# Kernel tuning notes

Hardware: AMD Instinct MI355X
Metric: run time of the kernel (lower is better)

The kernel has to match this reference:

```python
import jax, jax.numpy as jnp
import numpy as np

# Config constants (HNet300MConfig)
D = 1536          # d_model
H = 12            # n_heads // 2 used by chunk_attention
MAXC = 256        # max_chunks
MAXSEQ = 1024     # max_seq_length (size_embedding rows)
THRESH = 0.85     # boundary_threshold
B, S = 8, 1024


def setup_inputs() -> dict:
    key = jax.random.key(0)
    ks = jax.random.split(key, 10)
    def nrm(k, shape, scale=0.02):
        return jax.random.normal(k, shape, dtype=jnp.float32) * scale
    return {
        "x": jax.random.normal(ks[0], (B, S, D), dtype=jnp.float32),
        "boundaries": jax.random.uniform(ks[1], (B, S), dtype=jnp.float32),
        # nn.MultiheadAttention params
        "in_proj_w": nrm(ks[2], (3 * D, D)),
        "in_proj_b": jnp.zeros((3 * D,), jnp.float32),
        "out_w": nrm(ks[3], (D, D)),
        "out_b": jnp.zeros((D,), jnp.float32),
        # chunk_processor: Linear(D,2D) -> GELU -> Linear(2D,D) -> LayerNorm
        "w1": nrm(ks[4], (2 * D, D)),
        "b1": jnp.zeros((2 * D,), jnp.float32),
        "w2": nrm(ks[5], (D, 2 * D)),
        "b2": jnp.zeros((D,), jnp.float32),
        "ln_g": jnp.ones((D,), jnp.float32),
        "ln_b": jnp.zeros((D,), jnp.float32),
        "pos_enc": nrm(ks[6], (1, MAXC, D)),         # chunk_pos_encoding
        "size_emb": nrm(ks[7], (MAXSEQ, D), 1.0),    # size_embedding table
    }


def reference(x, boundaries, in_proj_w, in_proj_b, out_w, out_b,
              w1, b1, w2, b2, ln_g, ln_b, pos_enc, size_emb):
    dh = D // H
    # Chunk structure: boundary positions start chunks; seg_id = #boundaries up to
    # and including this token, minus 1. Tokens before the first boundary (seg=-1)
    # belong to no chunk. Final chunk runs from last boundary to seq end.
    is_b = boundaries > THRESH                                   # [B,S]
    seg = jnp.cumsum(is_b.astype(jnp.int32), axis=1) - 1         # [B,S]
    valid = seg >= 0

    # Per-chunk self-attention == full MHA with a block-diagonal mask.
    qkv = x @ in_proj_w.T + in_proj_b                            # [B,S,3D]
    q, k, v = jnp.split(qkv, 3, axis=-1)
    heads = lambda t: t.reshape(B, S, H, dh).transpose(0, 2, 1, 3)  # [B,H,S,dh]
    q, k, v = heads(q), heads(k), heads(v)
    scores = jnp.einsum('bhid,bhjd->bhij', q, k) / jnp.sqrt(jnp.float32(dh))
    blk = (seg[:, :, None] == seg[:, None, :]) & valid[:, :, None]  # [B,S,S]
    scores = jnp.where(blk[:, None], scores, jnp.float32(-1e9))
    attn = jax.nn.softmax(scores, axis=-1)
    ctx = jnp.einsum('bhij,bhjd->bhid', attn, v)
    ctx = ctx.transpose(0, 2, 1, 3).reshape(B, S, D)
    attn_out = ctx @ out_w.T + out_b                             # [B,S,D]

    # Ragged mean-pool per chunk (chunks beyond max_chunks are truncated;
    # tokens with seg=-1 or seg>=MAXC go to a dump bucket).
    seg_c = jnp.where(valid & (seg < MAXC), seg, MAXC)
    flat_seg = (seg_c + jnp.arange(B, dtype=jnp.int32)[:, None] * (MAXC + 1)).reshape(-1)
    sums = jax.ops.segment_sum(attn_out.reshape(-1, D), flat_seg,
                               num_segments=B * (MAXC + 1))
    cnts = jax.ops.segment_sum(jnp.ones((B * S,), jnp.float32), flat_seg,
                               num_segments=B * (MAXC + 1))
    sums = sums.reshape(B, MAXC + 1, D)[:, :MAXC]                # [B,MAXC,D]
    cnts = cnts.reshape(B, MAXC + 1)[:, :MAXC]                   # [B,MAXC]
    mean = sums / jnp.maximum(cnts, 1.0)[..., None]              # 0 for empty chunks

    # Size embedding added per non-empty chunk; empty (padding) chunks stay zero.
    lengths = cnts.astype(jnp.int32)
    size_idx = jnp.minimum(lengths, MAXSEQ - 1)
    size_vec = size_emb[size_idx] * (lengths > 0)[..., None].astype(jnp.float32)

    chunks = mean + size_vec + pos_enc                           # [B,MAXC,D]

    # chunk_processor (dropout inactive at inference)
    h = chunks @ w1.T + b1
    h = jax.nn.gelu(h, approximate=False)
    h = h @ w2.T + b2
    mu = jnp.mean(h, axis=-1, keepdims=True)
    var = jnp.mean((h - mu) ** 2, axis=-1, keepdims=True)
    out = (h - mu) / jnp.sqrt(var + 1e-5) * ln_g + ln_b
    return out
```

## Files before the change

### kernel.cpp

```cpp
#include <hip/hip_runtime.h>
#include <math.h>

#define NB 8
#define SEQ 1024
#define DM 1536
#define NHEAD 12
#define DHEAD 128
#define MAXC 256
#define QKVN 4608
#define THRESH 0.85f

typedef unsigned short u16;
typedef __attribute__((ext_vector_type(8))) __bf16 bf16x8;
typedef __attribute__((ext_vector_type(4))) float f32x4;

struct __align__(4) U2 { u16 x, y; };
struct __align__(8) U4 { u16 x, y, z, w; };

__device__ __forceinline__ float bf2f(u16 u) {
  union { unsigned i; float f; } c; c.i = ((unsigned)u) << 16; return c.f;
}
__device__ __forceinline__ u16 f2bf(float f) {
  union { float f; unsigned i; } c; c.f = f;
  unsigned r = c.i + 0x7FFFu + ((c.i >> 16) & 1u);
  return (u16)(r >> 16);
}

__global__ __launch_bounds__(256) void cvt5_bf16_kernel(
    const float* __restrict__ i0, u16* __restrict__ o0, int n0,
    const float* __restrict__ i1, u16* __restrict__ o1, int n1,
    const float* __restrict__ i2, u16* __restrict__ o2, int n2,
    const float* __restrict__ i3, u16* __restrict__ o3, int n3,
    const float* __restrict__ i4, u16* __restrict__ o4, int n4) {
  const int stride = gridDim.x * blockDim.x;
  const int t0 = blockIdx.x * blockDim.x + threadIdx.x;
  const float* ins[5] = {i0, i1, i2, i3, i4};
  u16* outs[5] = {o0, o1, o2, o3, o4};
  const int ns[5] = {n0, n1, n2, n3, n4};
#pragma unroll
  for (int a = 0; a < 5; ++a) {
    const float* in = ins[a];
    u16* out = outs[a];
    for (int i = t0; i < ns[a]; i += stride) {
      float4 f = ((const float4*)in)[i];
      U4 u; u.x = f2bf(f.x); u.y = f2bf(f.y); u.z = f2bf(f.z); u.w = f2bf(f.w);
      ((U4*)out)[i] = u;
    }
  }
}

__global__ __launch_bounds__(64) void segment_kernel(
    const float* __restrict__ bnd, int* __restrict__ nchunks,
    int* __restrict__ starts, int* __restrict__ lens) {
  const int b = blockIdx.x;
  const int lane = threadIdx.x;
  int running = 0;
  for (int g = 0; g < SEQ / 64; ++g) {
    int s = g * 64 + lane;
    bool isb = bnd[b * SEQ + s] > THRESH;
    unsigned long long mask = __ballot(isb ? 1 : 0);
    int excl = __popcll(mask & ((1ULL << lane) - 1ULL));
    if (isb) {
      int c = running + excl;
      if (c <= MAXC) starts[b * (MAXC + 1) + c] = s;
    }
    running += __popcll(mask);
  }
  if (lane == 0) nchunks[b] = running;
  __syncthreads();
  int ncl = min(running, MAXC);
  for (int c = lane; c < MAXC; c += 64) {
    int v = 0;
    if (c < ncl) {
      int st = starts[b * (MAXC + 1) + c];
      int en = (c + 1 < running) ? starts[b * (MAXC + 1) + c + 1] : SEQ;
      v = en - st;
    }
    lens[b * MAXC + c] = v;
  }
}

__global__ __launch_bounds__(512, 2) void gemm256_kernel(
    const u16* __restrict__ A, const u16* __restrict__ B,
    const int M, const int N, const int K,
    const float* __restrict__ bias, u16* __restrict__ outB) {
  __shared__ __align__(16) u16 lds[4][2][8192];
  const int tid = threadIdx.x;
  const int wid = tid >> 6;
  const int lane = tid & 63;
  const int cpx = gridDim.x >> 3;
  const int bid = ((int)blockIdx.x & 7) * cpx + ((int)blockIdx.x >> 3);
  const int NX = N >> 8;
  const int row0 = (bid / NX) << 8;
  const int col0 = (bid % NX) << 8;

  const int wr = wid >> 2;
  const int wc = wid & 3;
  const int rr = lane & 15;
  const int kg = lane >> 4;
  const int cw = rr * 4 + kg;
  const int slot = cw ^ ((cw >> 3) & 7);
  int srow[2], sk8[2];
#pragma unroll
  for (int i = 0; i < 2; ++i) {
    const int s = i * 512 + tid;
    const int g = s >> 6, c = s & 63;
    const int gch = c ^ ((c >> 3) & 7);
    srow[i] = g * 16 + (gch >> 2);
    sk8[i] = gch & 3;
  }

  const int NT = K >> 5;

#define STAGE(t)                                                              \
  {                                                                           \
    const int _b = (t) & 3;                                                   \
    const int _kb = (t) << 5;                                                 \
    _Pragma("unroll") for (int i = 0; i < 2; ++i) {                           \
      u16* ga = const_cast<u16*>(A) + (size_t)(row0 + srow[i]) * K + _kb +    \
                sk8[i] * 8;                                                   \
      u16* gb = const_cast<u16*>(B) + (size_t)(col0 + srow[i]) * K + _kb +    \
                sk8[i] * 8;                                                   \
      __builtin_amdgcn_global_load_lds(                                       \
          (__attribute__((address_space(1))) void*)ga,                        \
          (__attribute__((address_space(3))) void*)&lds[_b][0]                \
              [(i * 512 + wid * 64) * 8], 16, 0, 0);                          \
      __builtin_amdgcn_global_load_lds(                                       \
          (__attribute__((address_space(1))) void*)gb,                        \
          (__attribute__((address_space(3))) void*)&lds[_b][1]                \
              [(i * 512 + wid * 64) * 8], 16, 0, 0);                          \
    }                                                                         \
  }

  f32x4 acc[8][4] = {};

  STAGE(0); STAGE(1); STAGE(2);
  asm volatile("s_waitcnt vmcnt(8)" ::: "memory");
  __builtin_amdgcn_s_barrier();

  for (int t = 0; t < NT; ++t) {
    const int buf = t & 3;
    bf16x8 bf[4], af[8];
#pragma unroll
    for (int n = 0; n < 4; ++n)
      bf[n] = *(const bf16x8*)&lds[buf][1][((wc * 4 + n) * 64 + slot) * 8];
#pragma unroll
    for (int m = 0; m < 8; ++m)
      af[m] = *(const bf16x8*)&lds[buf][0][((wr * 8 + m) * 64 + slot) * 8];
    if (t + 3 < NT) STAGE(t + 3);
    __builtin_amdgcn_s_setprio(1);
#pragma unroll
    for (int m = 0; m < 8; ++m)
#pragma unroll
      for (int n = 0; n < 4; ++n)
        acc[m][n] = __builtin_amdgcn_mfma_f32_16x16x32_bf16(af[m], bf[n], acc[m][n], 0, 0, 0);
    __builtin_amdgcn_s_setprio(0);
    if (t + 3 < NT) {
      asm volatile("s_waitcnt vmcnt(8)" ::: "memory");
    } else if (t + 2 < NT) {
      asm volatile("s_waitcnt vmcnt(4)" ::: "memory");
    } else if (t + 1 < NT) {
      asm volatile("s_waitcnt vmcnt(0)" ::: "memory");
    }
    __builtin_amdgcn_s_barrier();
  }
#undef STAGE

#pragma unroll
  for (int m = 0; m < 8; ++m) {
#pragma unroll
    for (int n = 0; n < 4; ++n) {
      const int col = col0 + wc * 64 + n * 16 + rr;
      const float bs = bias[col];
#pragma unroll
      for (int j = 0; j < 4; ++j) {
        const int row = row0 + wr * 128 + m * 16 + (lane >> 4) * 4 + j;
        outB[(size_t)row * N + col] = f2bf(acc[m][n][j] + bs);
      }
    }
  }
}

template <int MODE>
__global__ __launch_bounds__(256) void gemm_bf16_kernel(
    const u16* __restrict__ A, const u16* __restrict__ B,
    const int M, const int N, const int K,
    const float* __restrict__ bias,
    u16* __restrict__ outB, float* __restrict__ outF,
    const int* __restrict__ lens, const float* __restrict__ semb,
    const float* __restrict__ pos) {
  __shared__ __align__(16) u16 As[2][128 * 32];
  __shared__ __align__(16) u16 Bs[2][128 * 32];
  const int tid = threadIdx.x;
  const int wave = tid >> 6;
  const int lane = tid & 63;
  const int row0 = blockIdx.y * 128;
  const int col0 = blockIdx.x * 128;
  const int wm = (wave >> 1) * 64;
  const int wn = (wave & 1) * 64;
  const int gch = lane ^ ((lane >> 3) & 7);
  const int sr = gch >> 2;
  const int sc = (gch & 3) * 8;
  const int rr = lane & 15;
  const int kg = lane >> 4;
  const int cwant = rr * 4 + kg;
  const int slot = cwant ^ ((cwant >> 3) & 7);
  const int NT = K >> 5;
  f32x4 acc[4][4] = {};

#define STAGE128(t, bb)                                                       \
  {                                                                           \
    const int _k = (t) << 5;                                                  \
    _Pragma("unroll") for (int tt = 0; tt < 2; ++tt) {                        \
      const int li = wave * 2 + tt;                                           \
      u16* ga = const_cast<u16*>(A) + (size_t)(row0 + li * 16 + sr) * K +     \
                _k + sc;                                                      \
      u16* gb = const_cast<u16*>(B) + (size_t)(col0 + li * 16 + sr) * K +     \
                _k + sc;                                                      \
      __builtin_amdgcn_global_load_lds(                                       \
          (__attribute__((address_space(1))) void*)ga,                        \
          (__attribute__((address_space(3))) void*)(As[bb] + li * 512), 16,   \
          0, 0);                                                              \
      __builtin_amdgcn_global_load_lds(                                       \
          (__attribute__((address_space(1))) void*)gb,                        \
          (__attribute__((address_space(3))) void*)(Bs[bb] + li * 512), 16,   \
          0, 0);                                                              \
    }                                                                         \
  }

  STAGE128(0, 0);
  asm volatile("s_waitcnt vmcnt(0)" ::: "memory");
  __builtin_amdgcn_s_barrier();

  for (int t = 0; t < NT; ++t) {
    const int cb = t & 1;
    bf16x8 bfr[4], af[4];
#pragma unroll
    for (int n = 0; n < 4; ++n)
      bfr[n] = *(const bf16x8*)(Bs[cb] + ((wn >> 4) + n) * 512 + slot * 8);
#pragma unroll
    for (int m = 0; m < 4; ++m)
      af[m] = *(const bf16x8*)(As[cb] + ((wm >> 4) + m) * 512 + slot * 8);
    if (t + 1 < NT) STAGE128(t + 1, cb ^ 1);
#pragma unroll
    for (int m = 0; m < 4; ++m)
#pragma unroll
      for (int n = 0; n < 4; ++n)
        acc[m][n] = __builtin_amdgcn_mfma_f32_16x16x32_bf16(af[m], bfr[n], acc[m][n], 0, 0, 0);
    if (t + 1 < NT) asm volatile("s_waitcnt vmcnt(0)" ::: "memory");
    __builtin_amdgcn_s_barrier();
  }
#undef STAGE128

  const int rg = (lane >> 4) * 4;
#pragma unroll
  for (int m = 0; m < 4; ++m) {
#pragma unroll
    for (int n = 0; n < 4; ++n) {
      const int col = col0 + wn + n * 16 + rr;
#pragma unroll
      for (int j = 0; j < 4; ++j) {
        const int row = row0 + wm + m * 16 + rg + j;
        float v = acc[m][n][j];
        if (MODE == 2) {
          const int len = lens[row];
          float val = 0.f;
          if (len > 0) {
            const int si = len < 1023 ? len : 1023;
            val = v + bias[col] + semb[(size_t)si * DM + col];
          }
          val += pos[(size_t)(row & (MAXC - 1)) * DM + col];
          outB[(size_t)row * N + col] = f2bf(val);
        } else if (MODE == 3) {
          float z = v + bias[col];
          float gel = 0.5f * z * (1.f + erff(z * 0.70710678118654752440f));
          outB[(size_t)row * N + col] = f2bf(gel);
        } else {
          outF[(size_t)row * N + col] = v + bias[col];
        }
      }
    }
  }
}

__global__ __launch_bounds__(64) void chunk_attn_kernel(
    const u16* __restrict__ qkv, const int* __restrict__ nchunks,
    const int* __restrict__ starts, const int* __restrict__ lens,
    u16* __restrict__ pooled) {
  __shared__ float g_lds[SEQ];
  const int h = blockIdx.x;
  const int c = blockIdx.y;
  const int b = blockIdx.z;
  const int lane = threadIdx.x;
  const int nc = min(nchunks[b], MAXC);
  u16* prow = pooled + ((size_t)(b * MAXC + c)) * DM + h * DHEAD;
  if (c >= nc) {
    U2 z; z.x = 0; z.y = 0;
    *(U2*)(prow + lane * 2) = z;
    return;
  }
  const int s0 = starts[b * (MAXC + 1) + c];
  const int L = lens[b * MAXC + c];
  const u16* Qb = qkv + ((size_t)(b * SEQ + s0)) * QKVN + h * DHEAD;
  const u16* Kb = Qb + DM;
  const u16* Vb = Qb + 2 * DM;

  const int col = lane & 15;
  const int grp = lane >> 4;
  const float scale = 0.08838834764831845f;
  const int half = lane >> 5;
  const int dl4 = (lane & 31) * 4;

  float a[4] = {0.f, 0.f, 0.f, 0.f};

  if (L <= 16) {
    const int rc = col < L ? col : (L - 1);
    bf16x8 qf[4], kf[4];
#pragma unroll
    for (int s = 0; s < 4; ++s) {
      qf[s] = *(const bf16x8*)(Qb + (size_t)rc * QKVN + s * 32 + grp * 8);
      kf[s] = *(const bf16x8*)(Kb + (size_t)rc * QKVN + s * 32 + grp * 8);
    }
    f32x4 sc = {0.f, 0.f, 0.f, 0.f};
#pragma unroll
    for (int s = 0; s < 4; ++s)
      sc = __builtin_amdgcn_mfma_f32_16x16x32_bf16(qf[s], kf[s], sc, 0, 0, 0);
    const bool kvalid = col < L;
    float g = 0.f;
#pragma unroll
    for (int j = 0; j < 4; ++j) {
      float sj = sc[j] * scale;
      float mv = kvalid ? sj : -3e38f;
      mv = fmaxf(mv, __shfl_xor(mv, 1));
      mv = fmaxf(mv, __shfl_xor(mv, 2));
      mv = fmaxf(mv, __shfl_xor(mv, 4));
      mv = fmaxf(mv, __shfl_xor(mv, 8));
      float pv = kvalid ? __expf(sj - mv) : 0.f;
      float dv = pv;
      dv += __shfl_xor(dv, 1);
      dv += __shfl_xor(dv, 2);
      dv += __shfl_xor(dv, 4);
      dv += __shfl_xor(dv, 8);
      const bool rv = (grp * 4 + j) < L;
      g += rv ? pv / dv : 0.f;
    }
    g += __shfl_xor(g, 16);
    g += __shfl_xor(g, 32);
    for (int j = 0; j < L; j += 2) {
      const int jj = j + half;
      const bool jv = jj < L;
      float gj = __shfl(g, jv ? jj : 0);
      if (!jv) gj = 0.f;
      const int jc = jv ? jj : 0;
      U4 vv = *(const U4*)(Vb + (size_t)jc * QKVN + dl4);
      a[0] += gj * bf2f(vv.x); a[1] += gj * bf2f(vv.y);
      a[2] += gj * bf2f(vv.z); a[3] += gj * bf2f(vv.w);
    }
  } else {
    float* gw = g_lds;
    for (int j = lane; j < L; j += 64) gw[j] = 0.f;
    const int NT = (L + 15) >> 4;
    for (int qt = 0; qt < NT; ++qt) {
      const int qr = qt * 16 + col;
      const int qrc = qr < L ? qr : (L - 1);
      bf16x8 qf[4];
#pragma unroll
      for (int s = 0; s < 4; ++s)
        qf[s] = *(const bf16x8*)(Qb + (size_t)qrc * QKVN + s * 32 + grp * 8);

      float m[4] = {-3e38f, -3e38f, -3e38f, -3e38f};
      float den[4] = {0.f, 0.f, 0.f, 0.f};
      for (int kt = 0; kt < NT; ++kt) {
        const int kr = kt * 16 + col;
        const bool kvalid = kr < L;
        const int krc = kvalid ? kr : (L - 1);
        f32x4 sc = {0.f, 0.f, 0.f, 0.f};
#pragma unroll
        for (int s = 0; s < 4; ++s) {
          bf16x8 kf = *(const bf16x8*)(Kb + (size_t)krc * QKVN + s * 32 + grp * 8);
          sc = __builtin_amdgcn_mfma_f32_16x16x32_bf16(qf[s], kf, sc, 0, 0, 0);
        }
#pragma unroll
        for (int j = 0; j < 4; ++j) {
          float sj = sc[j] * scale;
          float mv = kvalid ? sj : -3e38f;
          mv = fmaxf(mv, __shfl_xor(mv, 1));
          mv = fmaxf(mv, __shfl_xor(mv, 2));
          mv = fmaxf(mv, __shfl_xor(mv, 4));
          mv = fmaxf(mv, __shfl_xor(mv, 8));
          float mn = fmaxf(m[j], mv);
          float pv = kvalid ? __expf(sj - mn) : 0.f;
          pv += __shfl_xor(pv, 1);
          pv += __shfl_xor(pv, 2);
          pv += __shfl_xor(pv, 4);
          pv += __shfl_xor(pv, 8);
          den[j] = den[j] * __expf(m[j] - mn) + pv;
          m[j] = mn;
        }
      }
      float inv[4];
#pragma unroll
      for (int j = 0; j < 4; ++j) {
        const bool rv = (qt * 16 + grp * 4 + j) < L;
        inv[j] = rv ? 1.f / den[j] : 0.f;
      }
      for (int kt = 0; kt < NT; ++kt) {
        const int kr = kt * 16 + col;
        const bool kvalid = kr < L;
        const int krc = kvalid ? kr : (L - 1);
        f32x4 sc = {0.f, 0.f, 0.f, 0.f};
#pragma unroll
        for (int s = 0; s < 4; ++s) {
          bf16x8 kf = *(const bf16x8*)(Kb + (size_t)krc * QKVN + s * 32 + grp * 8);
          sc = __builtin_amdgcn_mfma_f32_16x16x32_bf16(qf[s], kf, sc, 0, 0, 0);
        }
        float colsum = 0.f;
#pragma unroll
        for (int j = 0; j < 4; ++j)
          colsum += __expf(sc[j] * scale - m[j]) * inv[j];
        colsum += __shfl_xor(colsum, 16);
        colsum += __shfl_xor(colsum, 32);
        if (grp == 0 && kvalid) gw[kt * 16 + col] += colsum;
      }
    }
    for (int j = 0; j < L; j += 2) {
      const int jj = j + half;
      const bool jv = jj < L;
      float gj = jv ? gw[jj] : 0.f;
      const int jc = jv ? jj : 0;
      U4 vv = *(const U4*)(Vb + (size_t)jc * QKVN + dl4);
      a[0] += gj * bf2f(vv.x); a[1] += gj * bf2f(vv.y);
      a[2] += gj * bf2f(vv.z); a[3] += gj * bf2f(vv.w);
    }
  }
  const float invL = 1.f / (float)L;
#pragma unroll
  for (int i = 0; i < 4; ++i) {
    a[i] += __shfl_xor(a[i], 32);
    a[i] *= invL;
  }
  if (lane < 32) {
    U4 r; r.x = f2bf(a[0]); r.y = f2bf(a[1]); r.z = f2bf(a[2]); r.w = f2bf(a[3]);
    *(U4*)(prow + dl4) = r;
  }
}

__global__ __launch_bounds__(256) void ln_kernel(
    const float* __restrict__ h2, const float* __restrict__ gamma,
    const float* __restrict__ beta, float* __restrict__ out) {
  const int row = blockIdx.x;
  const float* x = h2 + (size_t)row * DM;
  float* o = out + (size_t)row * DM;
  const int tid = threadIdx.x;
  float v[6];
  float s = 0.f;
#pragma unroll
  for (int i = 0; i < 6; ++i) { v[i] = x[tid + i * 256]; s += v[i]; }
  __shared__ float red[8];
#pragma unroll
  for (int off = 32; off; off >>= 1) s += __shfl_xor(s, off);
  if ((tid & 63) == 0) red[tid >> 6] = s;
  __syncthreads();
  const float mu = (red[0] + red[1] + red[2] + red[3]) * (1.f / (float)DM);
  float vs = 0.f;
#pragma unroll
  for (int i = 0; i < 6; ++i) { float d = v[i] - mu; vs += d * d; }
#pragma unroll
  for (int off = 32; off; off >>= 1) vs += __shfl_xor(vs, off);
  __shared__ float red2[8];
  if ((tid & 63) == 0) red2[tid >> 6] = vs;
  __syncthreads();
  const float var = (red2[0] + red2[1] + red2[2] + red2[3]) * (1.f / (float)DM);
  const float inv = rsqrtf(var + 1e-5f);
#pragma unroll
  for (int i = 0; i < 6; ++i) {
    const int cidx = tid + i * 256;
    o[cidx] = (v[i] - mu) * inv * gamma[cidx] + beta[cidx];
  }
}

extern "C" void kernel_launch(void* const* d_in, const int* in_sizes, int n_in,
                              void* d_out, int out_size, void* d_ws, size_t ws_size,
                              hipStream_t stream) {
  const float* x    = (const float*)d_in[0];
  const float* bnd  = (const float*)d_in[1];
  const float* wqkv = (const float*)d_in[2];
  const float* bqkv = (const float*)d_in[3];
  const float* wout = (const float*)d_in[4];
  const float* bout = (const float*)d_in[5];
  const float* w1   = (const float*)d_in[6];
  const float* b1   = (const float*)d_in[7];
  const float* w2   = (const float*)d_in[8];
  const float* b2   = (const float*)d_in[9];
  const float* lng  = (const float*)d_in[10];
  const float* lnb  = (const float*)d_in[11];
  const float* pos  = (const float*)d_in[12];
  const float* semb = (const float*)d_in[13];
  float* out = (float*)d_out;

  char* ws = (char*)d_ws;
  size_t off = 0;
  auto alloc = [&](size_t bytes) -> char* {
    char* p = ws + off;
    off += (bytes + 255) & ~(size_t)255;
    return p;
  };
  u16* x_bf    = (u16*)alloc((size_t)NB * SEQ * DM * 2);
  u16* wqkv_bf = (u16*)alloc((size_t)3 * DM * DM * 2);
  u16* wout_bf = (u16*)alloc((size_t)DM * DM * 2);
  u16* w1_bf   = (u16*)alloc((size_t)2 * DM * DM * 2);
  u16* w2_bf   = (u16*)alloc((size_t)2 * DM * DM * 2);
  u16* qkv_bf  = (u16*)alloc((size_t)NB * SEQ * QKVN * 2);
  int* nchunks = (int*)alloc(NB * 4);
  int* starts  = (int*)alloc(NB * (MAXC + 1) * 4);
  int* lens    = (int*)alloc(NB * MAXC * 4);
  u16* pooled  = (u16*)alloc((size_t)NB * MAXC * DM * 2);
  u16* chunks  = (u16*)alloc((size_t)NB * MAXC * DM * 2);
  u16* h1      = (u16*)alloc((size_t)NB * MAXC * 2 * DM * 2);
  float* h2    = (float*)alloc((size_t)NB * MAXC * DM * 4);
  (void)ws_size; (void)in_sizes; (void)n_in; (void)out_size;

  cvt5_bf16_kernel<<<2048, 256, 0, stream>>>(
      x, x_bf, NB * SEQ * DM / 4,
      wqkv, wqkv_bf, 3 * DM * DM / 4,
      wout, wout_bf, DM * DM / 4,
      w1, w1_bf, 2 * DM * DM / 4,
      w2, w2_bf, 2 * DM * DM / 4);

  segment_kernel<<<NB, 64, 0, stream>>>(bnd, nchunks, starts, lens);

  gemm256_kernel<<<(NB * SEQ / 256) * (QKVN / 256), 512, 0, stream>>>(
      x_bf, wqkv_bf, NB * SEQ, QKVN, DM, bqkv, qkv_bf);

  chunk_attn_kernel<<<dim3(NHEAD, MAXC, NB), 64, 0, stream>>>(
      qkv_bf, nchunks, starts, lens, pooled);

  gemm_bf16_kernel<2><<<dim3(DM / 128, NB * MAXC / 128), 256, 0, stream>>>(
      pooled, wout_bf, NB * MAXC, DM, DM, bout, chunks, nullptr, lens, semb, pos);

  gemm_bf16_kernel<3><<<dim3(2 * DM / 128, NB * MAXC / 128), 256, 0, stream>>>(
      chunks, w1_bf, NB * MAXC, 2 * DM, DM, b1, h1, nullptr, nullptr, nullptr, nullptr);

  gemm_bf16_kernel<4><<<dim3(DM / 128, NB * MAXC / 128), 256, 0, stream>>>(
      h1, w2_bf, NB * MAXC, DM, 2 * DM, b2, nullptr, h2, nullptr, nullptr, nullptr);

  ln_kernel<<<NB * MAXC, 256, 0, stream>>>(h2, lng, lnb, out);
}
```

Baseline: 352.5 us.

## Shrink QKV GEMM tile to 128x256 with 3-stage pipeline; triple-buffer chunk GEMMs

The QKV projection GEMM moves from 256x256 tiles with a 4-deep LDS ring to 128x256 tiles with a 3-deep ring. This halves per-wave accumulators and LDS use, so up to 4 blocks per CU can be resident and the grid doubles. The smaller chunk-level GEMMs go from double to triple buffering, with loads issued two iterations ahead and waitcnt values adjusted. The trade-off is less operand reuse per tile in the QKV GEMM, which means more global and LDS traffic per FLOP.

```diff
diff --git a/kernel.cpp b/kernel.cpp
--- a/kernel.cpp
+++ b/kernel.cpp
@@ -80,18 +80,18 @@
   }
 }
 
-__global__ __launch_bounds__(512, 2) void gemm256_kernel(
+__global__ __launch_bounds__(512, 4) void gemmQKV_kernel(
     const u16* __restrict__ A, const u16* __restrict__ B,
     const int M, const int N, const int K,
     const float* __restrict__ bias, u16* __restrict__ outB) {
-  __shared__ __align__(16) u16 lds[4][2][8192];
+  __shared__ __align__(16) u16 lds[3][12288];
   const int tid = threadIdx.x;
   const int wid = tid >> 6;
   const int lane = tid & 63;
   const int cpx = gridDim.x >> 3;
   const int bid = ((int)blockIdx.x & 7) * cpx + ((int)blockIdx.x >> 3);
   const int NX = N >> 8;
-  const int row0 = (bid / NX) << 8;
+  const int row0 = (bid / NX) << 7;
   const int col0 = (bid % NX) << 8;
 
   const int wr = wid >> 2;
@@ -100,65 +100,65 @@
   const int kg = lane >> 4;
   const int cw = rr * 4 + kg;
   const int slot = cw ^ ((cw >> 3) & 7);
-  int srow[2], sk8[2];
+  int srA, skA;
+  { const int c = tid & 63; const int g = tid >> 6;
+    const int gc = c ^ ((c >> 3) & 7);
+    srA = g * 16 + (gc >> 2); skA = (gc & 3) * 8; }
+  int srB[2], skB[2];
 #pragma unroll
   for (int i = 0; i < 2; ++i) {
     const int s = i * 512 + tid;
-    const int g = s >> 6, c = s & 63;
-    const int gch = c ^ ((c >> 3) & 7);
-    srow[i] = g * 16 + (gch >> 2);
-    sk8[i] = gch & 3;
+    const int c = s & 63; const int g = s >> 6;
+    const int gc = c ^ ((c >> 3) & 7);
+    srB[i] = g * 16 + (gc >> 2); skB[i] = (gc & 3) * 8;
   }
 
   const int NT = K >> 5;
 
 #define STAGE(t)                                                              \
   {                                                                           \
-    const int _b = (t) & 3;                                                   \
+    const int _b = (t) % 3;                                                   \
     const int _kb = (t) << 5;                                                 \
+    u16* ga = const_cast<u16*>(A) + (size_t)(row0 + srA) * K + _kb + skA;     \
+    __builtin_amdgcn_global_load_lds(                                         \
+        (__attribute__((address_space(1))) void*)ga,                          \
+        (__attribute__((address_space(3))) void*)&lds[_b][(wid * 64) * 8],    \
+        16, 0, 0);                                                            \
     _Pragma("unroll") for (int i = 0; i < 2; ++i) {                           \
-      u16* ga = const_cast<u16*>(A) + (size_t)(row0 + srow[i]) * K + _kb +    \
-                sk8[i] * 8;                                                   \
-      u16* gb = const_cast<u16*>(B) + (size_t)(col0 + srow[i]) * K + _kb +    \
-                sk8[i] * 8;                                                   \
-      __builtin_amdgcn_global_load_lds(                                       \
-          (__attribute__((address_space(1))) void*)ga,                        \
-          (__attribute__((address_space(3))) void*)&lds[_b][0]                \
-              [(i * 512 + wid * 64) * 8], 16, 0, 0);                          \
+      u16* gb = const_cast<u16*>(B) + (size_t)(col0 + srB[i]) * K + _kb +     \
+                skB[i];                                                       \
       __builtin_amdgcn_global_load_lds(                                       \
           (__attribute__((address_space(1))) void*)gb,                        \
-          (__attribute__((address_space(3))) void*)&lds[_b][1]                \
-              [(i * 512 + wid * 64) * 8], 16, 0, 0);                          \
+          (__attribute__((address_space(3))) void*)&lds[_b]                   \
+              [4096 + (i * 512 + wid * 64) * 8], 16, 0, 0);                   \
     }                                                                         \
   }
 
-  f32x4 acc[8][4] = {};
-
-  STAGE(0); STAGE(1); STAGE(2);
-  asm volatile("s_waitcnt vmcnt(8)" ::: "memory");
+  f32x4 acc[4][4] = {};
+
+  STAGE(0); STAGE(1);
+  asm volatile("s_waitcnt vmcnt(3)" ::: "memory");
   __builtin_amdgcn_s_barrier();
 
   for (int t = 0; t < NT; ++t) {
-    const int buf = t & 3;
-    bf16x8 bf[4], af[8];
+    const int buf = t % 3;
+    bf16x8 bf[4], af[4];
 #pragma unroll
     for (int n = 0; n < 4; ++n)
-      bf[n] = *(const bf16x8*)&lds[buf][1][((wc * 4 + n) * 64 + slot) * 8];
-#pragma unroll
-    for (int m = 0; m < 8; ++m)
-      af[m] = *(const bf16x8*)&lds[buf][0][((wr * 8 + m) * 64 + slot) * 8];
-    if (t + 3 < NT) STAGE(t + 3);
+      bf[n] = *(const bf16x8*)&lds[buf][4096 + ((wc * 4 + n) * 64 + slot) * 8];
+#pragma unroll
+    for (int m = 0; m < 4; ++m)
+      af[m] = *(const bf16x8*)&lds[buf][((wr * 4 + m) * 64 + slot) * 8];
+    if (t + 2 < NT) STAGE(t + 2);
     __builtin_amdgcn_s_setprio(1);
 #pragma unroll
-    for (int m = 0; m < 8; ++m)
+    for (int m = 0; m < 4; ++m)
 #pragma unroll
       for (int n = 0; n < 4; ++n)
         acc[m][n] = __builtin_amdgcn_mfma_f32_16x16x32_bf16(af[m], bf[n], acc[m][n], 0, 0, 0);
     __builtin_amdgcn_s_setprio(0);
-    if (t + 3 < NT) {
-      asm volatile("s_waitcnt vmcnt(8)" ::: "memory");
-    } else if (t + 2 < NT) {
-      asm volatile("s_waitcnt vmcnt(4)" ::: "memory");
+    if (t + 2 < NT) {
+      asm volatile("s_waitcnt vmcnt(3)" ::: "memory");
     } else if (t + 1 < NT) {
       asm volatile("s_waitcnt vmcnt(0)" ::: "memory");
     }
@@ -167,14 +167,14 @@
 #undef STAGE
 
 #pragma unroll
-  for (int m = 0; m < 8; ++m) {
+  for (int m = 0; m < 4; ++m) {
 #pragma unroll
     for (int n = 0; n < 4; ++n) {
       const int col = col0 + wc * 64 + n * 16 + rr;
       const float bs = bias[col];
 #pragma unroll
       for (int j = 0; j < 4; ++j) {
-        const int row = row0 + wr * 128 + m * 16 + (lane >> 4) * 4 + j;
+        const int row = row0 + wr * 64 + m * 16 + (lane >> 4) * 4 + j;
         outB[(size_t)row * N + col] = f2bf(acc[m][n][j] + bs);
       }
     }
@@ -189,8 +189,8 @@
     u16* __restrict__ outB, float* __restrict__ outF,
     const int* __restrict__ lens, const float* __restrict__ semb,
     const float* __restrict__ pos) {
-  __shared__ __align__(16) u16 As[2][128 * 32];
-  __shared__ __align__(16) u16 Bs[2][128 * 32];
+  __shared__ __align__(16) u16 As[3][128 * 32];
+  __shared__ __align__(16) u16 Bs[3][128 * 32];
   const int tid = threadIdx.x;
   const int wave = tid >> 6;
   const int lane = tid & 63;
@@ -208,8 +208,9 @@
   const int NT = K >> 5;
   f32x4 acc[4][4] = {};
 
-#define STAGE128(t, bb)                                                       \
+#define STAGE128(t)                                                           \
   {                                                                           \
+    const int _b = (t) % 3;                                                   \
     const int _k = (t) << 5;                                                  \
     _Pragma("unroll") for (int tt = 0; tt < 2; ++tt) {                        \
       const int li = wave * 2 + tt;                                           \
@@ -219,21 +220,21 @@
                 _k + sc;                                                      \
       __builtin_amdgcn_global_load_lds(                                       \
           (__attribute__((address_space(1))) void*)ga,                        \
-          (__attribute__((address_space(3))) void*)(As[bb] + li * 512), 16,   \
+          (__attribute__((address_space(3))) void*)(As[_b] + li * 512), 16,   \
           0, 0);                                                              \
       __builtin_amdgcn_global_load_lds(                                       \
           (__attribute__((address_space(1))) void*)gb,                        \
-          (__attribute__((address_space(3))) void*)(Bs[bb] + li * 512), 16,   \
+          (__attribute__((address_space(3))) void*)(Bs[_b] + li * 512), 16,   \
           0, 0);                                                              \
     }                                                                         \
   }
 
-  STAGE128(0, 0);
-  asm volatile("s_waitcnt vmcnt(0)" ::: "memory");
+  STAGE128(0); STAGE128(1);
+  asm volatile("s_waitcnt vmcnt(4)" ::: "memory");
   __builtin_amdgcn_s_barrier();
 
   for (int t = 0; t < NT; ++t) {
-    const int cb = t & 1;
+    const int cb = t % 3;
     bf16x8 bfr[4], af[4];
 #pragma unroll
     for (int n = 0; n < 4; ++n)
@@ -241,13 +242,17 @@
 #pragma unroll
     for (int m = 0; m < 4; ++m)
       af[m] = *(const bf16x8*)(As[cb] + ((wm >> 4) + m) * 512 + slot * 8);
-    if (t + 1 < NT) STAGE128(t + 1, cb ^ 1);
+    if (t + 2 < NT) STAGE128(t + 2);
 #pragma unroll
     for (int m = 0; m < 4; ++m)
 #pragma unroll
       for (int n = 0; n < 4; ++n)
         acc[m][n] = __builtin_amdgcn_mfma_f32_16x16x32_bf16(af[m], bfr[n], acc[m][n], 0, 0, 0);
-    if (t + 1 < NT) asm volatile("s_waitcnt vmcnt(0)" ::: "memory");
+    if (t + 2 < NT) {
+      asm volatile("s_waitcnt vmcnt(4)" ::: "memory");
+    } else if (t + 1 < NT) {
+      asm volatile("s_waitcnt vmcnt(0)" ::: "memory");
+    }
     __builtin_amdgcn_s_barrier();
   }
 #undef STAGE128
@@ -529,7 +534,7 @@
 
   segment_kernel<<<NB, 64, 0, stream>>>(bnd, nchunks, starts, lens);
 
-  gemm256_kernel<<<(NB * SEQ / 256) * (QKVN / 256), 512, 0, stream>>>(
+  gemmQKV_kernel<<<(NB * SEQ / 128) * (QKVN / 256), 512, 0, stream>>>(
       x_bf, wqkv_bf, NB * SEQ, QKVN, DM, bqkv, qkv_bf);
 
   chunk_attn_kernel<<<dim3(NHEAD, MAXC, NB), 64, 0, stream>>>(
```

After: 345.0 us. -2.1%, faster.
